# Performance work log

Hardware: AMD Instinct MI355X
Metric: run time of the kernel (lower is better)

The kernel has to match this reference:

```python
import jax, jax.numpy as jnp
import numpy as np

SHAPES = ((64, 64), (32, 32), (16, 16), (8, 8))
LEVEL_STARTS = np.concatenate([[0], np.cumsum([h * w for h, w in SHAPES])]).tolist()
N_LEVELS = 4; N_HEADS = 8; N_POINTS = 4; D_MODEL = 256; HEAD_DIM = 32; D_FFN = 1024; NUM_LAYERS = 2
LEN_IN = sum(h * w for h, w in SHAPES)
BATCH = 2


def setup_inputs():
    key = jax.random.key(0)
    ks = iter(jax.random.split(key, 40))
    r = lambda shape, s=1.0: jax.random.normal(next(ks), shape, dtype=jnp.float32) * s
    L = NUM_LAYERS
    return {
        "src": r((BATCH, LEN_IN, D_MODEL)),
        "pos": r((BATCH, LEN_IN, D_MODEL), 0.5),
        "valid_ratios": jnp.ones((BATCH, N_LEVELS, 2), jnp.float32),
        "Wv": r((L, D_MODEL, D_MODEL), 0.05), "bv": jnp.zeros((L, D_MODEL), jnp.float32),
        "Woff": r((L, D_MODEL, N_HEADS * N_LEVELS * N_POINTS * 2), 0.002),
        "boff": r((L, N_HEADS * N_LEVELS * N_POINTS * 2), 0.5),
        "Wa": r((L, D_MODEL, N_HEADS * N_LEVELS * N_POINTS), 0.05),
        "ba": jnp.zeros((L, N_HEADS * N_LEVELS * N_POINTS), jnp.float32),
        "Wo": r((L, D_MODEL, D_MODEL), 0.05), "bo": jnp.zeros((L, D_MODEL), jnp.float32),
        "g1": jnp.ones((L, D_MODEL), jnp.float32), "be1": jnp.zeros((L, D_MODEL), jnp.float32),
        "Wl1": r((L, D_MODEL, D_FFN), 0.05), "bl1": jnp.zeros((L, D_FFN), jnp.float32),
        "Wl2": r((L, D_FFN, D_MODEL), 0.05), "bl2": jnp.zeros((L, D_MODEL), jnp.float32),
        "g2": jnp.ones((L, D_MODEL), jnp.float32), "be2": jnp.zeros((L, D_MODEL), jnp.float32),
    }


def layer_norm(x, g, b, eps=1e-5):
    m = jnp.mean(x, -1, keepdims=True)
    v = jnp.mean(jnp.square(x - m), -1, keepdims=True)
    return (x - m) * jax.lax.rsqrt(v + eps) * g + b


def make_reference_points(valid_ratios):
    # DeformableTransformerEncoder.get_reference_points, vectorized per level
    refs = []
    for lvl, (H, W) in enumerate(SHAPES):
        gy, gx = jnp.meshgrid(jnp.arange(H, dtype=jnp.float32) + 0.5,
                              jnp.arange(W, dtype=jnp.float32) + 0.5, indexing="ij")
        ry = gy.reshape(-1)[None] / (valid_ratios[:, lvl, 1][:, None] * H)
        rx = gx.reshape(-1)[None] / (valid_ratios[:, lvl, 0][:, None] * W)
        refs.append(jnp.stack([rx, ry], -1))  # [N, H*W, 2]
    ref = jnp.concatenate(refs, 1)  # [N, Len, 2]
    return ref[:, :, None, :] * valid_ratios[:, None]  # [N, Len, n_levels, 2]


def ms_deform_attn(query, input_flatten, reference_points, Wv, bv, Woff, boff, Wa, ba, Wo, bo):
    N, Lq, _ = query.shape
    value = (input_flatten @ Wv + bv).reshape(N, -1, N_HEADS, HEAD_DIM)
    off = (query @ Woff + boff).reshape(N, Lq, N_HEADS, N_LEVELS, N_POINTS, 2)
    aw = (query @ Wa + ba).reshape(N, Lq, N_HEADS, N_LEVELS * N_POINTS)
    aw = jax.nn.softmax(aw, -1).reshape(N, Lq, N_HEADS, N_LEVELS, N_POINTS)
    # normalizer is (W, H) per level, as in MSDeformAttn
    normalizer = jnp.array([[w, h] for h, w in SHAPES], jnp.float32)
    loc = reference_points[:, :, None, :, None, :] + off / normalizer[None, None, None, :, None, :]
    acc = jnp.zeros((N, N_HEADS, Lq, HEAD_DIM), query.dtype)
    for lvl, (H, W) in enumerate(SHAPES):
        s = LEVEL_STARTS[lvl]
        val = value[:, s:s + H * W].transpose(0, 2, 1, 3)  # [N, heads, H*W, hd]
        # grid_sample bilinear, align_corners=False, zero padding
        x = loc[:, :, :, lvl, :, 0] * W - 0.5  # [N, Lq, heads, P]
        y = loc[:, :, :, lvl, :, 1] * H - 0.5
        x0 = jnp.floor(x); y0 = jnp.floor(y)
        wx1 = x - x0; wy1 = y - y0
        ix0 = x0.astype(jnp.int32); iy0 = y0.astype(jnp.int32)

        def corner(ix, iy, w):
            valid = (ix >= 0) & (ix < W) & (iy >= 0) & (iy < H)
            idx = jnp.clip(iy, 0, H - 1) * W + jnp.clip(ix, 0, W - 1)
            idx = idx.transpose(0, 2, 1, 3).reshape(N, N_HEADS, Lq * N_POINTS)
            g = jnp.take_along_axis(val, idx[..., None], axis=2).reshape(N, N_HEADS, Lq, N_POINTS, HEAD_DIM)
            w = jnp.where(valid, w, 0.0).transpose(0, 2, 1, 3)  # [N, heads, Lq, P]
            return g * w[..., None]

        sampled = (corner(ix0, iy0, (1 - wx1) * (1 - wy1))
                   + corner(ix0 + 1, iy0, wx1 * (1 - wy1))
                   + corner(ix0, iy0 + 1, (1 - wx1) * wy1)
                   + corner(ix0 + 1, iy0 + 1, wx1 * wy1))
        acc = acc + (sampled * aw[:, :, :, lvl].transpose(0, 2, 1, 3)[..., None]).sum(3)
    out = acc.transpose(0, 2, 1, 3).reshape(N, Lq, D_MODEL)
    return out @ Wo + bo


def reference(src, pos, valid_ratios, Wv, bv, Woff, boff, Wa, ba, Wo, bo,
              g1, be1, Wl1, bl1, Wl2, bl2, g2, be2):
    ref_pts = make_reference_points(valid_ratios)
    out = src
    for l in range(NUM_LAYERS):
        q = out + pos  # with_pos_embed
        attn = ms_deform_attn(q, out, ref_pts, Wv[l], bv[l], Woff[l], boff[l],
                              Wa[l], ba[l], Wo[l], bo[l])
        out = layer_norm(out + attn, g1[l], be1[l])
        ffn = jax.nn.relu(out @ Wl1[l] + bl1[l]) @ Wl2[l] + bl2[l]
        out = layer_norm(out + ffn, g2[l], be2[l])
    return out
```

## Files before the change

### kernel.cpp

```cpp
#include <hip/hip_runtime.h>
#include <math.h>

#define LEN   5440
#define NB    2
#define MROWS (NB * LEN)
#define DM    256
#define NH    8
#define HD    32
#define NLV   4
#define NPT   4
#define DFFN  1024

typedef __attribute__((ext_vector_type(8))) short bf16x8;
typedef __attribute__((ext_vector_type(4))) short bf16x4;
typedef __attribute__((ext_vector_type(4))) float f32x4;

#define MFMA16 __builtin_amdgcn_mfma_f32_16x16x32_bf16

__device__ __forceinline__ short f2bf(float f) {
    union { float f; unsigned u; } cv; cv.f = f;
    unsigned r = cv.u + 0x7fffu + ((cv.u >> 16) & 1u);
    return (short)(r >> 16);
}
__device__ __forceinline__ float bf2f(short s) {
    union { unsigned u; float f; } cv;
    cv.u = ((unsigned)(unsigned short)s) << 16;
    return cv.f;
}

__global__ __launch_bounds__(256) void transpose_convert_all(
    const float* __restrict__ Wv,  const float* __restrict__ Woff,
    const float* __restrict__ Wa,  const float* __restrict__ Wo,
    const float* __restrict__ Wl1, const float* __restrict__ Wl2,
    short* __restrict__ out)
{
    int bx = blockIdx.x;
    int l  = bx / 736;
    int t  = bx % 736;
    const float* src; int K, N; long doff;
    if      (t < 64)  { src = Wv;   K = 256;  N = 256;  doff = 0;      }
    else if (t < 128) { src = Woff; K = 256;  N = 256;  doff = 65536;  t -= 64;  }
    else if (t < 160) { src = Wa;   K = 256;  N = 128;  doff = 131072; t -= 128; }
    else if (t < 224) { src = Wo;   K = 256;  N = 256;  doff = 163840; t -= 160; }
    else if (t < 480) { src = Wl1;  K = 256;  N = 1024; doff = 229376; t -= 224; }
    else              { src = Wl2;  K = 1024; N = 256;  doff = 491520; t -= 480; }
    src += (long)l * K * N;
    short* dst = out + (long)l * 753664 + doff;

    const int ntx = N / 32;
    const int n0 = (t % ntx) * 32, k0 = (t / ntx) * 32;

    __shared__ short T[32][33];
    const int tid = threadIdx.x;
    {
        const int n = tid & 31, kq = tid >> 5;
        #pragma unroll
        for (int i = 0; i < 4; ++i) {
            int k = kq * 4 + i;
            T[n][k] = f2bf(src[(long)(k0 + k) * N + n0 + n]);
        }
    }
    __syncthreads();
    {
        const int k = tid & 31, nq = tid >> 5;
        #pragma unroll
        for (int i = 0; i < 4; ++i) {
            int n = nq * 4 + i;
            dst[(long)(n0 + n) * K + k0 + k] = T[n][k];
        }
    }
}

__global__ __launch_bounds__(256) void convert_src(
    const float4* __restrict__ s4, const float4* __restrict__ p4,
    bf16x4* __restrict__ curb, bf16x4* __restrict__ qb)
{
    const int i = blockIdx.x * 256 + threadIdx.x;
    float4 s = s4[i], p = p4[i];
    bf16x4 c, q;
    c[0] = f2bf(s.x); c[1] = f2bf(s.y); c[2] = f2bf(s.z); c[3] = f2bf(s.w);
    q[0] = f2bf(s.x + p.x); q[1] = f2bf(s.y + p.y);
    q[2] = f2bf(s.z + p.z); q[3] = f2bf(s.w + p.w);
    curb[i] = c; qb[i] = q;
}

template <int BN, int RELU, int OMODE>
__device__ __forceinline__ void gemm_core128(
    short* As, short* Bs,
    const short* __restrict__ A, const short* __restrict__ Wt,
    const float* __restrict__ bias, float* __restrict__ Cf,
    short* __restrict__ Cb,
    int ldc, int m0, int wrow0, int ccol0, int K)
{
    constexpr int NF = BN / 32;
    constexpr int NBJ = BN / 64;
    const int t    = threadIdx.x;
    const int wave = t >> 6, lane = t & 63;
    const int wm   = (wave & 1) * 64;
    const int wn   = (wave >> 1) * (BN / 2);
    const int lm   = lane & 15;
    const int chkg = lane >> 4;
    const int srow = t >> 2;
    const int sc   = t & 3;

    f32x4 acc[4][NF] = {};
    bf16x8 ar[2], br[NBJ];

    #pragma unroll
    for (int j = 0; j < 2; ++j)
        ar[j] = *(const bf16x8*)(A + (long)(m0 + srow + 64 * j) * K + sc * 8);
    #pragma unroll
    for (int j = 0; j < NBJ; ++j)
        br[j] = *(const bf16x8*)(Wt + (long)(wrow0 + srow + 64 * j) * K + sc * 8);

    for (int k0 = 0; k0 < K; k0 += 32) {
        __syncthreads();
        #pragma unroll
        for (int j = 0; j < 2; ++j)
            *(bf16x8*)(&As[(srow + 64 * j) * 40 + sc * 8]) = ar[j];
        #pragma unroll
        for (int j = 0; j < NBJ; ++j)
            *(bf16x8*)(&Bs[(srow + 64 * j) * 40 + sc * 8]) = br[j];
        __syncthreads();

        if (k0 + 32 < K) {
            #pragma unroll
            for (int j = 0; j < 2; ++j)
                ar[j] = *(const bf16x8*)(A + (long)(m0 + srow + 64 * j) * K + k0 + 32 + sc * 8);
            #pragma unroll
            for (int j = 0; j < NBJ; ++j)
                br[j] = *(const bf16x8*)(Wt + (long)(wrow0 + srow + 64 * j) * K + k0 + 32 + sc * 8);
        }

        bf16x8 af[4], bfv[NF];
        #pragma unroll
        for (int s = 0; s < 4; ++s)
            af[s] = *(const bf16x8*)(&As[(wm + s * 16 + lm) * 40 + chkg * 8]);
        #pragma unroll
        for (int u = 0; u < NF; ++u)
            bfv[u] = *(const bf16x8*)(&Bs[(wn + u * 16 + lm) * 40 + chkg * 8]);
        #pragma unroll
        for (int s = 0; s < 4; ++s)
            #pragma unroll
            for (int u = 0; u < NF; ++u)
                acc[s][u] = MFMA16(af[s], bfv[u], acc[s][u], 0, 0, 0);
    }

    const int col = lane & 15;
    const int rq  = (lane >> 4) * 4;
    #pragma unroll
    for (int s = 0; s < 4; ++s) {
        #pragma unroll
        for (int u = 0; u < NF; ++u) {
            const int gn = ccol0 + wn + u * 16 + col;
            const float bb = bias[gn];
            #pragma unroll
            for (int r = 0; r < 4; ++r) {
                const int gm = m0 + wm + s * 16 + rq + r;
                float v = acc[s][u][r] + bb;
                if (RELU) v = fmaxf(v, 0.f);
                if (OMODE == 0) {
                    Cf[(long)gm * ldc + gn] = v;
                } else if (OMODE == 1) {
                    Cb[(long)gm * ldc + gn] = f2bf(v);
                } else {
                    const int n   = gm / LEN;
                    const int pix = gm - n * LEN;
                    const int h   = gn >> 5, d = gn & 31;
                    Cb[((long)(n * NH + h) * LEN + pix) * 32 + d] = f2bf(v);
                }
            }
        }
    }
}

template <int BN, int RELU, int OMODE>
__global__ __launch_bounds__(256) void gemm128(
    const short* __restrict__ A, const short* __restrict__ Wt,
    const float* __restrict__ bias, float* Cf, short* Cb, int ldc, int K)
{
    __shared__ __align__(16) short As[128 * 40];
    __shared__ __align__(16) short Bs[BN * 40];
    gemm_core128<BN, RELU, OMODE>(As, Bs, A, Wt, bias, Cf, Cb, ldc,
                                  blockIdx.y * 128, blockIdx.x * BN,
                                  blockIdx.x * BN, K);
}

__global__ __launch_bounds__(256) void gemm_qkv128(
    const short* __restrict__ curb, const short* __restrict__ qb,
    const short* __restrict__ Wt, const float* __restrict__ bv,
    const float* __restrict__ boff, const float* __restrict__ ba,
    short* __restrict__ Vb, float* __restrict__ OFF, float* __restrict__ AW)
{
    __shared__ __align__(16) short As[128 * 40];
    __shared__ __align__(16) short Bs[128 * 40];
    const int n0 = blockIdx.x * 128;
    if (n0 < 256) {
        gemm_core128<128, 0, 2>(As, Bs, curb, Wt, bv, (float*)nullptr, Vb,
                                256, blockIdx.y * 128, n0, n0, 256);
    } else if (n0 < 512) {
        gemm_core128<128, 0, 0>(As, Bs, qb, Wt, boff, OFF, (short*)nullptr,
                                256, blockIdx.y * 128, n0, n0 - 256, 256);
    } else {
        gemm_core128<128, 0, 0>(As, Bs, qb, Wt, ba, AW, (short*)nullptr,
                                128, blockIdx.y * 128, n0, n0 - 512, 256);
    }
}

template <int K>
__global__ __launch_bounds__(256) void gemm_ln(
    const short* __restrict__ A, const short* __restrict__ Wt,
    const float* __restrict__ bias, const short* __restrict__ residb,
    const float* __restrict__ g, const float* __restrict__ be,
    short* __restrict__ outb, short* __restrict__ outq,
    float* __restrict__ outf, const float* __restrict__ pos)
{
    __shared__ __align__(16) short As[32 * 40];
    __shared__ __align__(16) short Bs[256 * 40];
    __shared__ float red[2][32][2];

    const int t    = threadIdx.x;
    const int wave = t >> 6, lane = t & 63;
    const int wm   = (wave & 1) * 16;
    const int wn   = (wave >> 1) * 128;
    const int lm   = lane & 15;
    const int chkg = lane >> 4;
    const int rq   = chkg * 4;
    const int srow = t >> 2;
    const int sc   = t & 3;
    const int m0   = blockIdx.x * 32;
    const bool doA = (t < 128);

    short rr[8][4];
    #pragma unroll
    for (int u = 0; u < 8; ++u)
        #pragma unroll
        for (int r = 0; r < 4; ++r)
            rr[u][r] = residb[(long)(m0 + wm + rq + r) * DM + wn + u * 16 + lm];

    f32x4 acc[8] = {};
    bf16x8 ar, br[4];

    if (doA) ar = *(const bf16x8*)(A + (long)(m0 + srow) * K + sc * 8);
    #pragma unroll
    for (int j = 0; j < 4; ++j)
        br[j] = *(const bf16x8*)(Wt + (long)(srow + 64 * j) * K + sc * 8);

    for (int k0 = 0; k0 < K; k0 += 32) {
        __syncthreads();
        if (doA) *(bf16x8*)(&As[srow * 40 + sc * 8]) = ar;
        #pragma unroll
        for (int j = 0; j < 4; ++j)
            *(bf16x8*)(&Bs[(srow + 64 * j) * 40 + sc * 8]) = br[j];
        __syncthreads();

        if (k0 + 32 < K) {
            if (doA) ar = *(const bf16x8*)(A + (long)(m0 + srow) * K + k0 + 32 + sc * 8);
            #pragma unroll
            for (int j = 0; j < 4; ++j)
                br[j] = *(const bf16x8*)(Wt + (long)(srow + 64 * j) * K + k0 + 32 + sc * 8);
        }

        bf16x8 af = *(const bf16x8*)(&As[(wm + lm) * 40 + chkg * 8]);
        #pragma unroll
        for (int u = 0; u < 8; ++u) {
            bf16x8 bfv = *(const bf16x8*)(&Bs[(wn + u * 16 + lm) * 40 + chkg * 8]);
            acc[u] = MFMA16(af, bfv, acc[u], 0, 0, 0);
        }
    }

    #pragma unroll
    for (int u = 0; u < 8; ++u) {
        const int gn = wn + u * 16 + lm;
        const float bb = bias[gn];
        #pragma unroll
        for (int r = 0; r < 4; ++r)
            acc[u][r] += bb + bf2f(rr[u][r]);
    }

    float rs[4], r2[4];
    #pragma unroll
    for (int r = 0; r < 4; ++r) {
        float s = 0.f, s2 = 0.f;
        #pragma unroll
        for (int u = 0; u < 8; ++u) { const float v = acc[u][r]; s += v; s2 += v * v; }
        rs[r] = s; r2[r] = s2;
    }
    #pragma unroll
    for (int o = 1; o < 16; o <<= 1)
        #pragma unroll
        for (int r = 0; r < 4; ++r) {
            rs[r] += __shfl_xor(rs[r], o, 64);
            r2[r] += __shfl_xor(r2[r], o, 64);
        }
    if (lm == 0) {
        #pragma unroll
        for (int r = 0; r < 4; ++r) {
            red[wave >> 1][wm + rq + r][0] = rs[r];
            red[wave >> 1][wm + rq + r][1] = r2[r];
        }
    }
    __syncthreads();
    #pragma unroll
    for (int r = 0; r < 4; ++r) {
        const int row = wm + rq + r;
        const float ts = red[0][row][0] + red[1][row][0];
        const float t2 = red[0][row][1] + red[1][row][1];
        const float mean = ts * (1.f / DM);
        const float var  = t2 * (1.f / DM) - mean * mean;
        rs[r] = mean;
        r2[r] = rsqrtf(var + 1e-5f);
    }
    #pragma unroll
    for (int u = 0; u < 8; ++u) {
        const int gn = wn + u * 16 + lm;
        const float gg = g[gn], bbe = be[gn];
        #pragma unroll
        for (int r = 0; r < 4; ++r) {
            const long gm = m0 + wm + rq + r;
            const float o = (acc[u][r] - rs[r]) * r2[r] * gg + bbe;
            if (outb) outb[gm * DM + gn] = f2bf(o);
            if (outq) outq[gm * DM + gn] = f2bf(o + pos[gm * DM + gn]);
            if (outf) outf[gm * DM + gn] = o;
        }
    }
}

__global__ __launch_bounds__(256) void deform_attn_v3(
    const short* __restrict__ Vb,
    const float* __restrict__ OFF,
    const float* __restrict__ AW,
    const float* __restrict__ vr,
    bf16x4* __restrict__ ATTb)
{
    const int starts[5] = {0, 4096, 5120, 5376, 5440};
    const int dims[4]   = {64, 32, 16, 8};

    const int wave = threadIdx.x >> 6;
    const int lane = threadIdx.x & 63;
    const int h    = lane >> 3;
    const int d4   = lane & 7;

    const int gq = blockIdx.x * 4 + wave;
    const int n  = gq / LEN;
    const int q  = gq % LEN;

    int lq = 3;
    if (q < 4096) lq = 0; else if (q < 5120) lq = 1; else if (q < 5376) lq = 2;
    const int r  = q - starts[lq];
    const int Wq = dims[lq];
    const int gy = r / Wq, gx = r % Wq;
    const float vrxq = vr[(n * NLV + lq) * 2 + 0];
    const float vryq = vr[(n * NLV + lq) * 2 + 1];
    const float rx = (gx + 0.5f) / (vrxq * Wq);
    const float ry = (gy + 0.5f) / (vryq * Wq);

    const long row = (long)n * LEN + q;

    const float* awp = AW + row * 128 + h * 16;
    float a[16];
    float mx = -1e30f;
    #pragma unroll
    for (int i = 0; i < 16; ++i) { a[i] = awp[i]; mx = fmaxf(mx, a[i]); }
    float s = 0.f;
    #pragma unroll
    for (int i = 0; i < 16; ++i) { a[i] = __expf(a[i] - mx); s += a[i]; }
    const float inv = 1.f / s;

    const float* offp = OFF + row * 256 + h * 32;

    float4 acc = {0.f, 0.f, 0.f, 0.f};
    #pragma unroll
    for (int lvl = 0; lvl < NLV; ++lvl) {
        const int Hl = dims[lvl];
        const int Wl = Hl;
        const float fW = (float)Wl;
        const int sb = starts[lvl];
        const float lx = rx * vr[(n * NLV + lvl) * 2 + 0];
        const float ly = ry * vr[(n * NLV + lvl) * 2 + 1];
        const short* vb = Vb + ((long)(n * NH + h) * LEN + sb) * 32 + d4 * 4;
        #pragma unroll
        for (int p = 0; p < NPT; ++p) {
            const float ox = offp[lvl * 8 + p * 2 + 0];
            const float oy = offp[lvl * 8 + p * 2 + 1];
            const float x = fmaf(lx, fW, ox) - 0.5f;
            const float y = fmaf(ly, fW, oy) - 0.5f;
            const float x0f = floorf(x), y0f = floorf(y);
            const int ix0 = (int)x0f, iy0 = (int)y0f;
            const float wx1 = x - x0f, wy1 = y - y0f;
            const float wx0 = 1.f - wx1, wy0 = 1.f - wy1;

            const bool vx0 = (ix0 >= 0)     && (ix0 < Wl);
            const bool vx1 = (ix0 + 1 >= 0) && (ix0 + 1 < Wl);
            const bool vy0 = (iy0 >= 0)     && (iy0 < Hl);
            const bool vy1 = (iy0 + 1 >= 0) && (iy0 + 1 < Hl);
            const int cx0 = min(max(ix0, 0), Wl - 1);
            const int cx1 = min(max(ix0 + 1, 0), Wl - 1);
            const int cy0 = min(max(iy0, 0), Hl - 1);
            const int cy1 = min(max(iy0 + 1, 0), Hl - 1);

            const float w00 = (vx0 && vy0) ? wx0 * wy0 : 0.f;
            const float w10 = (vx1 && vy0) ? wx1 * wy0 : 0.f;
            const float w01 = (vx0 && vy1) ? wx0 * wy1 : 0.f;
            const float w11 = (vx1 && vy1) ? wx1 * wy1 : 0.f;

            const bf16x4 g00 = *(const bf16x4*)(vb + (long)(cy0 * Wl + cx0) * 32);
            const bf16x4 g10 = *(const bf16x4*)(vb + (long)(cy0 * Wl + cx1) * 32);
            const bf16x4 g01 = *(const bf16x4*)(vb + (long)(cy1 * Wl + cx0) * 32);
            const bf16x4 g11 = *(const bf16x4*)(vb + (long)(cy1 * Wl + cx1) * 32);

            const float awv = a[lvl * 4 + p] * inv;
            #pragma unroll
            for (int e = 0; e < 4; ++e) {
                float sv = w00 * bf2f(g00[e]) + w10 * bf2f(g10[e])
                         + w01 * bf2f(g01[e]) + w11 * bf2f(g11[e]);
                (&acc.x)[e] += awv * sv;
            }
        }
    }
    bf16x4 ob;
    ob[0] = f2bf(acc.x); ob[1] = f2bf(acc.y);
    ob[2] = f2bf(acc.z); ob[3] = f2bf(acc.w);
    ATTb[row * 64 + h * 8 + d4] = ob;
}

extern "C" void kernel_launch(void* const* d_in, const int* in_sizes, int n_in,
                              void* d_out, int out_size, void* d_ws, size_t ws_size,
                              hipStream_t stream)
{
    const float* src = (const float*)d_in[0];
    const float* pos = (const float*)d_in[1];
    const float* vr  = (const float*)d_in[2];
    const float* Wv_   = (const float*)d_in[3];
    const float* bv_   = (const float*)d_in[4];
    const float* Woff_ = (const float*)d_in[5];
    const float* boff_ = (const float*)d_in[6];
    const float* Wa_   = (const float*)d_in[7];
    const float* ba_   = (const float*)d_in[8];
    const float* Wo_   = (const float*)d_in[9];
    const float* bo_   = (const float*)d_in[10];
    const float* g1_   = (const float*)d_in[11];
    const float* be1_  = (const float*)d_in[12];
    const float* Wl1_  = (const float*)d_in[13];
    const float* bl1_  = (const float*)d_in[14];
    const float* Wl2_  = (const float*)d_in[15];
    const float* bl2_  = (const float*)d_in[16];
    const float* g2_   = (const float*)d_in[17];
    const float* be2_  = (const float*)d_in[18];

    const long SZ = (long)MROWS * DM;
    float* ws = (float*)d_ws;
    float* OFF  = ws;
    float* AW   = OFF + SZ;
    short* Vb   = (short*)(AW + (long)MROWS * 128);
    short* curb = Vb   + SZ;
    short* qb   = curb + SZ;
    short* ATTb = qb   + SZ;
    short* XAb  = ATTb + SZ;
    short* FFNb = XAb  + SZ;
    short* Wt   = FFNb + (long)MROWS * DFFN;

    const dim3 blk(256);
    const int GYM = MROWS / 128;
    const int GLN = MROWS / 32;

    hipLaunchKernelGGL(transpose_convert_all, dim3(1472), blk, 0, stream,
                       Wv_, Woff_, Wa_, Wo_, Wl1_, Wl2_, Wt);
    hipLaunchKernelGGL(convert_src, dim3(SZ / 4 / 256), blk, 0, stream,
                       (const float4*)src, (const float4*)pos,
                       (bf16x4*)curb, (bf16x4*)qb);

    for (int l = 0; l < 2; ++l) {
        const short* Wbase = Wt + (long)l * 753664;
        const float* bv   = bv_   + (long)l * DM;
        const float* boff = boff_ + (long)l * 256;
        const float* ba   = ba_   + (long)l * 128;
        const float* bo   = bo_   + (long)l * DM;
        const float* g1   = g1_   + (long)l * DM;
        const float* be1  = be1_  + (long)l * DM;
        const float* bl1  = bl1_  + (long)l * DFFN;
        const float* bl2  = bl2_  + (long)l * DM;
        const float* g2   = g2_   + (long)l * DM;
        const float* be2  = be2_  + (long)l * DM;

        hipLaunchKernelGGL(gemm_qkv128, dim3(5, GYM), blk, 0, stream,
                           curb, qb, Wbase, bv, boff, ba, Vb, OFF, AW);
        hipLaunchKernelGGL(deform_attn_v3, dim3(MROWS / 4), blk, 0, stream,
                           Vb, OFF, AW, vr, (bf16x4*)ATTb);
        hipLaunchKernelGGL((gemm_ln<256>), dim3(GLN), blk, 0, stream,
                           ATTb, Wbase + 163840, bo, curb, g1, be1,
                           XAb, (short*)nullptr, (float*)nullptr,
                           (const float*)nullptr);
        hipLaunchKernelGGL((gemm128<128, 1, 1>), dim3(8, GYM), blk, 0, stream,
                           XAb, Wbase + 229376, bl1, (float*)nullptr, FFNb, 1024, 256);
        if (l == 0) {
            hipLaunchKernelGGL((gemm_ln<1024>), dim3(GLN), blk, 0, stream,
                               FFNb, Wbase + 491520, bl2, XAb, g2, be2,
                               curb, qb, (float*)nullptr, pos);
        } else {
            hipLaunchKernelGGL((gemm_ln<1024>), dim3(GLN), blk, 0, stream,
                               FFNb, Wbase + 491520, bl2, XAb, g2, be2,
                               (short*)nullptr, (short*)nullptr,
                               (float*)d_out, (const float*)nullptr);
        }
    }
}
```

Before: 309.0 us.

## Use direct global-to-LDS loads with double-buffered swizzled tiles in GEMMs

Replaces the register-staged global→LDS copy in the GEMM cores (qkv, FFN1, and the LN-fused GEMMs) with global_load_lds 16-byte direct loads into double-buffered LDS tiles. It prefetches two k-tiles ahead, waits with explicit vmcnt counts, and uses an XOR swizzle instead of row padding to avoid bank conflicts. The goal is to overlap memory with MFMA work and free registers used for staging. It relies on hand-tuned waitcnt values and raw barriers, which are fragile if the instruction count per stage changes.

```diff
diff --git a/kernel.cpp b/kernel.cpp
--- a/kernel.cpp
+++ b/kernel.cpp
@@ -27,6 +27,19 @@
     cv.u = ((unsigned)(unsigned short)s) << 16;
     return cv.f;
 }
+
+__device__ __forceinline__ void gload16(const short* g, short* l) {
+    __builtin_amdgcn_global_load_lds(
+        (__attribute__((address_space(1))) void*)g,
+        (__attribute__((address_space(3))) void*)l, 16, 0, 0);
+}
+
+template <int N> __device__ __forceinline__ void vmwait();
+template <> __device__ __forceinline__ void vmwait<0>() { asm volatile("s_waitcnt vmcnt(0)" ::: "memory"); }
+template <> __device__ __forceinline__ void vmwait<4>() { asm volatile("s_waitcnt vmcnt(4)" ::: "memory"); }
+template <> __device__ __forceinline__ void vmwait<5>() { asm volatile("s_waitcnt vmcnt(5)" ::: "memory"); }
+
+__device__ __forceinline__ int swz(int row) { return (row >> 1) & 3; }
 
 __global__ __launch_bounds__(256) void transpose_convert_all(
     const float* __restrict__ Wv,  const float* __restrict__ Woff,
@@ -84,74 +97,95 @@
     curb[i] = c; qb[i] = q;
 }
 
-template <int BN, int RELU, int OMODE>
-__device__ __forceinline__ void gemm_core128(
+template <int RELU, int OMODE, int K>
+__device__ __forceinline__ void gemm_core128_v2(
     short* As, short* Bs,
     const short* __restrict__ A, const short* __restrict__ Wt,
     const float* __restrict__ bias, float* __restrict__ Cf,
-    short* __restrict__ Cb,
-    int ldc, int m0, int wrow0, int ccol0, int K)
-{
-    constexpr int NF = BN / 32;
-    constexpr int NBJ = BN / 64;
+    short* __restrict__ Cb, int ldc, int m0, int wrow0, int ccol0)
+{
+    constexpr int NT = K / 32;
+    static_assert(NT >= 4 && (NT & 1) == 0, "NT even >= 4");
     const int t    = threadIdx.x;
     const int wave = t >> 6, lane = t & 63;
     const int wm   = (wave & 1) * 64;
-    const int wn   = (wave >> 1) * (BN / 2);
+    const int wn   = (wave >> 1) * 64;
     const int lm   = lane & 15;
     const int chkg = lane >> 4;
-    const int srow = t >> 2;
-    const int sc   = t & 3;
-
-    f32x4 acc[4][NF] = {};
-    bf16x8 ar[2], br[NBJ];
-
-    #pragma unroll
-    for (int j = 0; j < 2; ++j)
-        ar[j] = *(const bf16x8*)(A + (long)(m0 + srow + 64 * j) * K + sc * 8);
-    #pragma unroll
-    for (int j = 0; j < NBJ; ++j)
-        br[j] = *(const bf16x8*)(Wt + (long)(wrow0 + srow + 64 * j) * K + sc * 8);
-
-    for (int k0 = 0; k0 < K; k0 += 32) {
-        __syncthreads();
-        #pragma unroll
-        for (int j = 0; j < 2; ++j)
-            *(bf16x8*)(&As[(srow + 64 * j) * 40 + sc * 8]) = ar[j];
-        #pragma unroll
-        for (int j = 0; j < NBJ; ++j)
-            *(bf16x8*)(&Bs[(srow + 64 * j) * 40 + sc * 8]) = br[j];
-        __syncthreads();
-
-        if (k0 + 32 < K) {
-            #pragma unroll
-            for (int j = 0; j < 2; ++j)
-                ar[j] = *(const bf16x8*)(A + (long)(m0 + srow + 64 * j) * K + k0 + 32 + sc * 8);
-            #pragma unroll
-            for (int j = 0; j < NBJ; ++j)
-                br[j] = *(const bf16x8*)(Wt + (long)(wrow0 + srow + 64 * j) * K + k0 + 32 + sc * 8);
-        }
-
-        bf16x8 af[4], bfv[NF];
-        #pragma unroll
-        for (int s = 0; s < 4; ++s)
-            af[s] = *(const bf16x8*)(&As[(wm + s * 16 + lm) * 40 + chkg * 8]);
-        #pragma unroll
-        for (int u = 0; u < NF; ++u)
-            bfv[u] = *(const bf16x8*)(&Bs[(wn + u * 16 + lm) * 40 + chkg * 8]);
-        #pragma unroll
-        for (int s = 0; s < 4; ++s)
-            #pragma unroll
-            for (int u = 0; u < NF; ++u)
-                acc[s][u] = MFMA16(af[s], bfv[u], acc[s][u], 0, 0, 0);
-    }
+
+    const short* aS[2]; const short* bS[2];
+    short *aD[2], *bD[2];
+    #pragma unroll
+    for (int i = 0; i < 2; ++i) {
+        const int c   = wave * 2 + i;
+        const int row = c * 16 + (lane >> 2);
+        const int xc  = (lane & 3) ^ swz(row);
+        aS[i] = A  + (long)(m0 + row) * K + xc * 8;
+        bS[i] = Wt + (long)(wrow0 + row) * K + xc * 8;
+        aD[i] = As + c * 512;
+        bD[i] = Bs + c * 512;
+    }
+
+    int offA[4], offB[4];
+    #pragma unroll
+    for (int s = 0; s < 4; ++s) {
+        const int r = wm + s * 16 + lm;
+        offA[s] = r * 32 + (chkg ^ swz(r)) * 8;
+    }
+    #pragma unroll
+    for (int u = 0; u < 4; ++u) {
+        const int r = wn + u * 16 + lm;
+        offB[u] = r * 32 + (chkg ^ swz(r)) * 8;
+    }
+
+    f32x4 acc[4][4] = {};
+
+#define STG128(BUF, KT) do {                                          \
+        const int _ko = (KT) * 32;                                    \
+        gload16(aS[0] + _ko, aD[0] + (BUF) * 4096);                   \
+        gload16(bS[0] + _ko, bD[0] + (BUF) * 4096);                   \
+        gload16(aS[1] + _ko, aD[1] + (BUF) * 4096);                   \
+        gload16(bS[1] + _ko, bD[1] + (BUF) * 4096);                   \
+    } while (0)
+
+#define GB128(T, BUF, WN, DOSTAGE) do {                               \
+        vmwait<WN>();                     \
+        __builtin_amdgcn_s_barrier();     \
+        bf16x8 af[4], bv[4];                                          \
+        _Pragma("unroll")                                             \
+        for (int s = 0; s < 4; ++s)                                   \
+            af[s] = *(const bf16x8*)(As + (BUF) * 4096 + offA[s]);    \
+        _Pragma("unroll")                                             \
+        for (int u = 0; u < 4; ++u)                                   \
+            bv[u] = *(const bf16x8*)(Bs + (BUF) * 4096 + offB[u]);    \
+        asm volatile("s_waitcnt lgkmcnt(0)" ::: "memory");            \
+        __builtin_amdgcn_s_barrier();     \
+        __builtin_amdgcn_sched_barrier(0);                            \
+        if (DOSTAGE) STG128(BUF, (T) + 2);                            \
+        _Pragma("unroll")                                             \
+        for (int s = 0; s < 4; ++s)                                   \
+            _Pragma("unroll")                                         \
+            for (int u = 0; u < 4; ++u)                               \
+                acc[s][u] = MFMA16(af[s], bv[u], acc[s][u], 0, 0, 0); \
+    } while (0)
+
+    STG128(0, 0);
+    STG128(1, 1);
+    for (int tt = 0; tt < NT - 2; tt += 2) {
+        GB128(tt,     0, 4, true);
+        GB128(tt + 1, 1, 4, true);
+    }
+    GB128(NT - 2, 0, 4, false);
+    GB128(NT - 1, 1, 0, false);
+#undef GB128
+#undef STG128
 
     const int col = lane & 15;
     const int rq  = (lane >> 4) * 4;
     #pragma unroll
     for (int s = 0; s < 4; ++s) {
         #pragma unroll
-        for (int u = 0; u < NF; ++u) {
+        for (int u = 0; u < 4; ++u) {
             const int gn = ccol0 + wn + u * 16 + col;
             const float bb = bias[gn];
             #pragma unroll
@@ -174,16 +208,16 @@
     }
 }
 
-template <int BN, int RELU, int OMODE>
-__global__ __launch_bounds__(256) void gemm128(
+template <int RELU, int OMODE, int K>
+__global__ __launch_bounds__(256) void gemm128v2(
     const short* __restrict__ A, const short* __restrict__ Wt,
-    const float* __restrict__ bias, float* Cf, short* Cb, int ldc, int K)
-{
-    __shared__ __align__(16) short As[128 * 40];
-    __shared__ __align__(16) short Bs[BN * 40];
-    gemm_core128<BN, RELU, OMODE>(As, Bs, A, Wt, bias, Cf, Cb, ldc,
-                                  blockIdx.y * 128, blockIdx.x * BN,
-                                  blockIdx.x * BN, K);
+    const float* __restrict__ bias, float* Cf, short* Cb, int ldc)
+{
+    __shared__ __align__(16) short As[2 * 128 * 32];
+    __shared__ __align__(16) short Bs[2 * 128 * 32];
+    gemm_core128_v2<RELU, OMODE, K>(As, Bs, A, Wt, bias, Cf, Cb, ldc,
+                                    blockIdx.y * 128, blockIdx.x * 128,
+                                    blockIdx.x * 128);
 }
 
 __global__ __launch_bounds__(256) void gemm_qkv128(
@@ -192,18 +226,18 @@
     const float* __restrict__ boff, const float* __restrict__ ba,
     short* __restrict__ Vb, float* __restrict__ OFF, float* __restrict__ AW)
 {
-    __shared__ __align__(16) short As[128 * 40];
-    __shared__ __align__(16) short Bs[128 * 40];
+    __shared__ __align__(16) short As[2 * 128 * 32];
+    __shared__ __align__(16) short Bs[2 * 128 * 32];
     const int n0 = blockIdx.x * 128;
     if (n0 < 256) {
-        gemm_core128<128, 0, 2>(As, Bs, curb, Wt, bv, (float*)nullptr, Vb,
-                                256, blockIdx.y * 128, n0, n0, 256);
+        gemm_core128_v2<0, 2, 256>(As, Bs, curb, Wt, bv, (float*)nullptr, Vb,
+                                   256, blockIdx.y * 128, n0, n0);
     } else if (n0 < 512) {
-        gemm_core128<128, 0, 0>(As, Bs, qb, Wt, boff, OFF, (short*)nullptr,
-                                256, blockIdx.y * 128, n0, n0 - 256, 256);
+        gemm_core128_v2<0, 0, 256>(As, Bs, qb, Wt, boff, OFF, (short*)nullptr,
+                                   256, blockIdx.y * 128, n0, n0 - 256);
     } else {
-        gemm_core128<128, 0, 0>(As, Bs, qb, Wt, ba, AW, (short*)nullptr,
-                                128, blockIdx.y * 128, n0, n0 - 512, 256);
+        gemm_core128_v2<0, 0, 256>(As, Bs, qb, Wt, ba, AW, (short*)nullptr,
+                                   128, blockIdx.y * 128, n0, n0 - 512);
     }
 }
 
@@ -215,8 +249,9 @@
     short* __restrict__ outb, short* __restrict__ outq,
     float* __restrict__ outf, const float* __restrict__ pos)
 {
-    __shared__ __align__(16) short As[32 * 40];
-    __shared__ __align__(16) short Bs[256 * 40];
+    constexpr int NT = K / 32;
+    __shared__ __align__(16) short As[2 * 32 * 32];
+    __shared__ __align__(16) short Bs[2 * 256 * 32];
     __shared__ float red[2][32][2];
 
     const int t    = threadIdx.x;
@@ -226,10 +261,8 @@
     const int lm   = lane & 15;
     const int chkg = lane >> 4;
     const int rq   = chkg * 4;
-    const int srow = t >> 2;
-    const int sc   = t & 3;
     const int m0   = blockIdx.x * 32;
-    const bool doA = (t < 128);
+    const bool hasA = (wave & 1) == 0;
 
     short rr[8][4];
     #pragma unroll
@@ -237,37 +270,72 @@
         #pragma unroll
         for (int r = 0; r < 4; ++r)
             rr[u][r] = residb[(long)(m0 + wm + rq + r) * DM + wn + u * 16 + lm];
+    asm volatile("" ::: "memory");
+
+    const short* bSp[4]; short* bDp[4];
+    #pragma unroll
+    for (int i = 0; i < 4; ++i) {
+        const int c   = wave * 4 + i;
+        const int row = c * 16 + (lane >> 2);
+        const int xc  = (lane & 3) ^ swz(row);
+        bSp[i] = Wt + (long)row * K + xc * 8;
+        bDp[i] = Bs + c * 512;
+    }
+    const short* aSp = nullptr; short* aDp = nullptr;
+    if (hasA) {
+        const int c   = wave >> 1;
+        const int row = c * 16 + (lane >> 2);
+        const int xc  = (lane & 3) ^ swz(row);
+        aSp = A + (long)(m0 + row) * K + xc * 8;
+        aDp = As + c * 512;
+    }
+
+    const int offA = (wm + lm) * 32 + (chkg ^ swz(wm + lm)) * 8;
+    int offB[8];
+    #pragma unroll
+    for (int u = 0; u < 8; ++u) {
+        const int r = wn + u * 16 + lm;
+        offB[u] = r * 32 + (chkg ^ swz(r)) * 8;
+    }
 
     f32x4 acc[8] = {};
-    bf16x8 ar, br[4];
-
-    if (doA) ar = *(const bf16x8*)(A + (long)(m0 + srow) * K + sc * 8);
-    #pragma unroll
-    for (int j = 0; j < 4; ++j)
-        br[j] = *(const bf16x8*)(Wt + (long)(srow + 64 * j) * K + sc * 8);
-
-    for (int k0 = 0; k0 < K; k0 += 32) {
-        __syncthreads();
-        if (doA) *(bf16x8*)(&As[srow * 40 + sc * 8]) = ar;
-        #pragma unroll
-        for (int j = 0; j < 4; ++j)
-            *(bf16x8*)(&Bs[(srow + 64 * j) * 40 + sc * 8]) = br[j];
-        __syncthreads();
-
-        if (k0 + 32 < K) {
-            if (doA) ar = *(const bf16x8*)(A + (long)(m0 + srow) * K + k0 + 32 + sc * 8);
-            #pragma unroll
-            for (int j = 0; j < 4; ++j)
-                br[j] = *(const bf16x8*)(Wt + (long)(srow + 64 * j) * K + k0 + 32 + sc * 8);
-        }
-
-        bf16x8 af = *(const bf16x8*)(&As[(wm + lm) * 40 + chkg * 8]);
-        #pragma unroll
-        for (int u = 0; u < 8; ++u) {
-            bf16x8 bfv = *(const bf16x8*)(&Bs[(wn + u * 16 + lm) * 40 + chkg * 8]);
-            acc[u] = MFMA16(af, bfv, acc[u], 0, 0, 0);
-        }
-    }
+
+#define STGLN(BUF, KT) do {                                           \
+        const int _ko = (KT) * 32;                                    \
+        if (hasA) gload16(aSp + _ko, aDp + (BUF) * 1024);             \
+        gload16(bSp[0] + _ko, bDp[0] + (BUF) * 8192);                 \
+        gload16(bSp[1] + _ko, bDp[1] + (BUF) * 8192);                 \
+        gload16(bSp[2] + _ko, bDp[2] + (BUF) * 8192);                 \
+        gload16(bSp[3] + _ko, bDp[3] + (BUF) * 8192);                 \
+    } while (0)
+
+#define GBLN(T, BUF, WA, WB, DOSTAGE) do {                            \
+        if (hasA) vmwait<WA>(); else vmwait<WB>();                    \
+        __builtin_amdgcn_s_barrier();                                 \
+        bf16x8 af = *(const bf16x8*)(As + (BUF) * 1024 + offA);       \
+        bf16x8 bv[8];                                                 \
+        _Pragma("unroll")                                             \
+        for (int u = 0; u < 8; ++u)                                   \
+            bv[u] = *(const bf16x8*)(Bs + (BUF) * 8192 + offB[u]);    \
+        asm volatile("s_waitcnt lgkmcnt(0)" ::: "memory");            \
+        __builtin_amdgcn_s_barrier();                                 \
+        __builtin_amdgcn_sched_barrier(0);                            \
+        if (DOSTAGE) STGLN(BUF, (T) + 2);                             \
+        _Pragma("unroll")                                             \
+        for (int u = 0; u < 8; ++u)                                   \
+            acc[u] = MFMA16(af, bv[u], acc[u], 0, 0, 0);              \
+    } while (0)
+
+    STGLN(0, 0);
+    STGLN(1, 1);
+    for (int tt = 0; tt < NT - 2; tt += 2) {
+        GBLN(tt,     0, 5, 4, true);
+        GBLN(tt + 1, 1, 5, 4, true);
+    }
+    GBLN(NT - 2, 0, 5, 4, false);
+    GBLN(NT - 1, 1, 0, 0, false);
+#undef GBLN
+#undef STGLN
 
     #pragma unroll
     for (int u = 0; u < 8; ++u) {
@@ -491,8 +559,8 @@
                            ATTb, Wbase + 163840, bo, curb, g1, be1,
                            XAb, (short*)nullptr, (float*)nullptr,
                            (const float*)nullptr);
-        hipLaunchKernelGGL((gemm128<128, 1, 1>), dim3(8, GYM), blk, 0, stream,
-                           XAb, Wbase + 229376, bl1, (float*)nullptr, FFNb, 1024, 256);
+        hipLaunchKernelGGL((gemm128v2<1, 1, 256>), dim3(8, GYM), blk, 0, stream,
+                           XAb, Wbase + 229376, bl1, (float*)nullptr, FFNb, 1024);
         if (l == 0) {
             hipLaunchKernelGGL((gemm_ln<1024>), dim3(GLN), blk, 0, stream,
                                FFNb, Wbase + 491520, bl2, XAb, g2, be2,
```

Result: faster. 291.9 us (-5.5%).
